# Performance work log

Measured on AMD Instinct MI355X. Metric: run time of the kernel, lower is better.

Reference implementation:

```python
import jax, jax.numpy as jnp
import numpy as np

NQ, NK, D = 8192, 8192, 128

def setup_inputs() -> dict:
    key = jax.random.key(0)
    kq, kk, kv = jax.random.split(key, 3)
    Q = jax.random.normal(kq, (NQ, D), dtype=jnp.float32)
    K = jax.random.normal(kk, (NK, D), dtype=jnp.float32)
    V = jax.random.normal(kv, (NK, D), dtype=jnp.float32)
    return {"Q": Q, "K": K, "V": V}

def reference(Q, K, V):
    d_k = K.shape[-1]
    scores = jnp.matmul(Q, K.T) / jnp.sqrt(jnp.asarray(d_k, Q.dtype))  # [NQ, NK]
    probs = jax.nn.softmax(scores, axis=-1)  # softmax over key axis
    return jnp.matmul(probs, V)  # [NQ, D]
```

## Files before the change

### kernel.cpp

```cpp
#include <hip/hip_runtime.h>
#include <hip/hip_bf16.h>

#define NQ 8192
#define NK 8192
#define DH 128
#define KVBLK 64
#define SLICES 8
#define TILES (NK / SLICES / KVBLK)
#define LOG2E 1.44269504088896340736f

typedef __attribute__((ext_vector_type(8))) short short8;
typedef __attribute__((ext_vector_type(8))) unsigned short ushort8v;
typedef __attribute__((ext_vector_type(16))) float f32x16;

static __device__ __forceinline__ unsigned short f2bf(float x){
  unsigned u = __builtin_bit_cast(unsigned, x);
  u += 0x7FFFu + ((u >> 16) & 1u);
  return (unsigned short)(u >> 16);
}

static __device__ __forceinline__ void gload_lds16(const void* g, void* l){
  __builtin_amdgcn_global_load_lds((const __attribute__((address_space(1))) void*)g,
                                   (__attribute__((address_space(3))) void*)l,
                                   16, 0, 0);
}

__global__ __launch_bounds__(512) void prep_q(const float4* __restrict__ Q4,
                                              ushort8v* __restrict__ Qb8)
{
  int i = blockIdx.x * 512 + threadIdx.x;
  const float s = 0.08838834764831844f;
  float4 a = Q4[2 * i], b = Q4[2 * i + 1];
  ushort8v o;
  o[0]=f2bf(a.x*s); o[1]=f2bf(a.y*s); o[2]=f2bf(a.z*s); o[3]=f2bf(a.w*s);
  o[4]=f2bf(b.x*s); o[5]=f2bf(b.y*s); o[6]=f2bf(b.z*s); o[7]=f2bf(b.w*s);
  Qb8[i] = o;
}

__global__ __launch_bounds__(512) void prep_kv(const float* __restrict__ K,
                                               const float* __restrict__ V,
                                               unsigned char* __restrict__ Kt,
                                               unsigned char* __restrict__ Vt)
{
  __shared__ float vs[KVBLK * DH];
  const int tile = blockIdx.x;
  const int tid  = threadIdx.x;

  const float4* Vg = (const float4*)(V + (size_t)tile * KVBLK * DH);
  float4* vs4 = (float4*)vs;
#pragma unroll
  for (int k = 0; k < 4; ++k) vs4[tid + k * 512] = Vg[tid + k * 512];

  unsigned char* Ktb = Kt + (size_t)tile * 16384;
  const float* Kg = K + (size_t)tile * KVBLK * DH;
#pragma unroll
  for (int k = 0; k < 2; ++k){
    int task = tid + k * 512;
    int kv = task >> 4, d0 = (task & 15) * 8;
    const float4* p = (const float4*)(Kg + kv * DH + d0);
    float4 a = p[0], b = p[1];
    ushort8v o;
    o[0]=f2bf(a.x); o[1]=f2bf(a.y); o[2]=f2bf(a.z); o[3]=f2bf(a.w);
    o[4]=f2bf(b.x); o[5]=f2bf(b.y); o[6]=f2bf(b.z); o[7]=f2bf(b.w);
    int addr = (kv * 256 + d0 * 2) ^ ((kv & 7) << 4);
    *(ushort8v*)(Ktb + addr) = o;
  }
  __syncthreads();

  unsigned char* Vtb = Vt + (size_t)tile * 16384;
#pragma unroll
  for (int k = 0; k < 2; ++k){
    int task = tid + k * 512;
    int d = task >> 3, mm = (task >> 1) & 3, h = task & 1;
    int kvb = mm * 16 + h * 4;
    ushort8v o;
    o[0]=f2bf(vs[(kvb+0)*DH + d]); o[1]=f2bf(vs[(kvb+1)*DH + d]);
    o[2]=f2bf(vs[(kvb+2)*DH + d]); o[3]=f2bf(vs[(kvb+3)*DH + d]);
    o[4]=f2bf(vs[(kvb+8)*DH + d]); o[5]=f2bf(vs[(kvb+9)*DH + d]);
    o[6]=f2bf(vs[(kvb+10)*DH + d]); o[7]=f2bf(vs[(kvb+11)*DH + d]);
    int addr = (d * 128 + (mm * 16 + h * 8) * 2) ^ ((d & 7) << 4);
    *(ushort8v*)(Vtb + addr) = o;
  }
}

__global__ __launch_bounds__(512, 2) void attn_kernel(
    const unsigned short* __restrict__ Qb,
    const unsigned char* __restrict__ Kt,
    const unsigned char* __restrict__ Vt,
    float* __restrict__ Opart, float* __restrict__ Mpart, float* __restrict__ Lpart)
{
  __shared__ unsigned char lK[2][16384];
  __shared__ unsigned char lV[2][16384];

  const int tid  = threadIdx.x;
  const int wave = tid >> 6;
  const int lane = tid & 63;
  const int l32  = lane & 31;
  const int h    = lane >> 5;
  const int bq    = blockIdx.x >> 3;
  const int slice = blockIdx.x & 7;
  const int qrow0 = bq * 256 + wave * 32;
  const size_t tile0 = (size_t)slice * TILES;
  const int kx = (l32 & 7) << 4;

  short8 qf[8];
  {
    const unsigned short* qp = Qb + (size_t)(qrow0 + l32) * DH + 8 * h;
#pragma unroll
    for (int m = 0; m < 8; ++m) qf[m] = *(const short8*)(qp + 16 * m);
  }

  f32x16 acc[4];
#pragma unroll
  for (int c = 0; c < 4; ++c)
#pragma unroll
    for (int r = 0; r < 16; ++r) acc[c][r] = 0.0f;
  float m_run = -3.0e38f, l_run = 0.0f;

  auto stage = [&](int buf, int t){
    if (wave < 4){
      const unsigned char* g = Kt + (tile0 + t) * 16384 + (wave * 64 + lane) * 16;
      unsigned char* l = &lK[buf][(wave * 64 + lane) * 16];
#pragma unroll
      for (int j = 0; j < 4; ++j) gload_lds16(g + j * 4096, l + j * 4096);
    } else {
      const unsigned char* g = Vt + (tile0 + t) * 16384 + ((wave - 4) * 64 + lane) * 16;
      unsigned char* l = &lV[buf][((wave - 4) * 64 + lane) * 16];
#pragma unroll
      for (int j = 0; j < 4; ++j) gload_lds16(g + j * 4096, l + j * 4096);
    }
  };

  stage(0, 0);
  __syncthreads();
  int cur = 0;

  for (int t = 0; t < TILES; ++t){
    if (t + 1 < TILES) stage(cur ^ 1, t + 1);

    const unsigned char* Kb = lK[cur];
    const unsigned char* Vb = lV[cur];

    f32x16 S0, S1;
#pragma unroll
    for (int r = 0; r < 16; ++r){ S0[r] = 0.0f; S1[r] = 0.0f; }
    __builtin_amdgcn_s_setprio(1);
#pragma unroll
    for (int m = 0; m < 8; ++m){
      short8 a = *(const short8*)(Kb + l32 * 256 + ((32 * m + 16 * h) ^ kx));
      short8 b = *(const short8*)(Kb + 8192 + l32 * 256 + ((32 * m + 16 * h) ^ kx));
      S0 = __builtin_amdgcn_mfma_f32_32x32x16_bf16(a, qf[m], S0, 0, 0, 0);
      S1 = __builtin_amdgcn_mfma_f32_32x32x16_bf16(b, qf[m], S1, 0, 0, 0);
    }
    __builtin_amdgcn_s_setprio(0);

    float pm = -3.0e38f;
#pragma unroll
    for (int r = 0; r < 16; ++r){
      pm = fmaxf(pm, S0[r]);
      pm = fmaxf(pm, S1[r]);
    }
    pm = fmaxf(pm, __shfl_xor(pm, 32, 64));

    if (!__all(pm <= m_run + 8.0f)){
      float mnew = fmaxf(m_run, pm);
      float rs = exp2f((m_run - mnew) * LOG2E);
      l_run *= rs; m_run = mnew;
#pragma unroll
      for (int r = 0; r < 16; ++r){
        float f = __shfl(rs, (r & 3) + 8 * (r >> 2) + 4 * h, 64);
#pragma unroll
        for (int c = 0; c < 4; ++c) acc[c][r] *= f;
      }
    }

    float p0[16], p1[16], psum = 0.0f;
#pragma unroll
    for (int r = 0; r < 16; ++r){
      p0[r] = exp2f((S0[r] - m_run) * LOG2E);
      p1[r] = exp2f((S1[r] - m_run) * LOG2E);
      psum += p0[r] + p1[r];
    }
    psum += __shfl_xor(psum, 32, 64);
    l_run += psum;

    short8 pa[4];
#pragma unroll
    for (int e = 0; e < 8; ++e){
      pa[0][e] = (short)f2bf(p0[e]);
      pa[1][e] = (short)f2bf(p0[8 + e]);
      pa[2][e] = (short)f2bf(p1[e]);
      pa[3][e] = (short)f2bf(p1[8 + e]);
    }

    __builtin_amdgcn_s_setprio(1);
#pragma unroll
    for (int c = 0; c < 4; ++c){
      const unsigned char* vrow = Vb + (32 * c + l32) * 128;
#pragma unroll
      for (int mm = 0; mm < 4; ++mm){
        short8 vfr = *(const short8*)(vrow + ((mm * 32 + 16 * h) ^ kx));
        acc[c] = __builtin_amdgcn_mfma_f32_32x32x16_bf16(pa[mm], vfr, acc[c], 0, 0, 0);
      }
    }
    __builtin_amdgcn_s_setprio(0);

    __syncthreads();
    cur ^= 1;
  }

  if (lane < 32){
    Mpart[(size_t)slice * NQ + qrow0 + lane] = m_run;
    Lpart[(size_t)slice * NQ + qrow0 + lane] = l_run;
  }
#pragma unroll
  for (int c = 0; c < 4; ++c)
#pragma unroll
    for (int r = 0; r < 16; ++r){
      int q = qrow0 + (r & 3) + 8 * (r >> 2) + 4 * h;
      Opart[((size_t)slice * NQ + q) * DH + 32 * c + l32] = acc[c][r];
    }
}

__global__ __launch_bounds__(256) void combine_kernel(
    const float4* __restrict__ Op4, const float* __restrict__ Mp,
    const float* __restrict__ Lp, float4* __restrict__ Out4)
{
  const int q  = blockIdx.x * 8 + (threadIdx.x >> 5);
  const int dd = threadIdx.x & 31;

  float ms[SLICES], M = -3.0e38f;
#pragma unroll
  for (int s = 0; s < SLICES; ++s){ ms[s] = Mp[s * NQ + q]; M = fmaxf(M, ms[s]); }
  float L = 0.0f, w[SLICES];
#pragma unroll
  for (int s = 0; s < SLICES; ++s){
    w[s] = exp2f((ms[s] - M) * LOG2E);
    L += Lp[s * NQ + q] * w[s];
  }
  float4 o = make_float4(0.f, 0.f, 0.f, 0.f);
#pragma unroll
  for (int s = 0; s < SLICES; ++s){
    float4 v = Op4[((size_t)s * NQ + q) * 32 + dd];
    o.x += w[s] * v.x; o.y += w[s] * v.y; o.z += w[s] * v.z; o.w += w[s] * v.w;
  }
  float inv = 1.0f / L;
  Out4[(size_t)q * 32 + dd] = make_float4(o.x * inv, o.y * inv, o.z * inv, o.w * inv);
}

extern "C" void kernel_launch(void* const* d_in, const int* in_sizes, int n_in,
                              void* d_out, int out_size, void* d_ws, size_t ws_size,
                              hipStream_t stream)
{
  const float* Q = (const float*)d_in[0];
  const float* K = (const float*)d_in[1];
  const float* V = (const float*)d_in[2];

  unsigned char* ws = (unsigned char*)d_ws;
  const size_t MB2 = (size_t)NQ * DH * 2;
  unsigned short* Qb = (unsigned short*)ws;
  unsigned char*  Kt = ws + MB2;
  unsigned char*  Vt = ws + 2 * MB2;
  float* Mp = (float*)(ws + 3 * MB2);
  float* Lp = Mp + (size_t)SLICES * NQ;
  float* Op = Lp + (size_t)SLICES * NQ;

  prep_q<<<NQ * DH / 8 / 512, 512, 0, stream>>>((const float4*)Q, (ushort8v*)Qb);
  prep_kv<<<NK / KVBLK, 512, 0, stream>>>(K, V, Kt, Vt);
  attn_kernel<<<(NQ / 256) * SLICES, 512, 0, stream>>>(Qb, Kt, Vt, Op, Mp, Lp);
  combine_kernel<<<NQ / 8, 256, 0, stream>>>((const float4*)Op, Mp, Lp, (float4*)d_out);
}
```

Baseline: 125.2 us.

## Give each wave 64 query rows, halve KV tiles, double slices, store bf16 partials

Each wave now computes two 32-row query blocks that share every K and V fragment loaded from LDS. This halves LDS reads per MFMA. KV tiles shrink to 32 rows and the key split grows to 16 slices with 256-thread blocks, and the staging and swizzle layout are rewritten to match. The log2e factor is folded into the Q prescale so the per-element multiplies in the exponentials go away. Partial outputs are written as bf16 to cut workspace traffic into the combine kernel, which adds rounding error and doubles the number of partials to merge.

```diff
diff --git a/kernel.cpp b/kernel.cpp
--- a/kernel.cpp
+++ b/kernel.cpp
@@ -4,10 +4,11 @@
 #define NQ 8192
 #define NK 8192
 #define DH 128
-#define KVBLK 64
-#define SLICES 8
-#define TILES (NK / SLICES / KVBLK)
-#define LOG2E 1.44269504088896340736f
+#define KVBLK 32
+#define SLICES 16
+#define KVPER (NK / SLICES)
+#define TILES (KVPER / KVBLK)
+#define NTILES (NK / KVBLK)
 
 typedef __attribute__((ext_vector_type(8))) short short8;
 typedef __attribute__((ext_vector_type(8))) unsigned short ushort8v;
@@ -18,7 +19,10 @@
   u += 0x7FFFu + ((u >> 16) & 1u);
   return (unsigned short)(u >> 16);
 }
-
+static __device__ __forceinline__ float bf2f(unsigned short x){
+  unsigned u = ((unsigned)x) << 16;
+  return __builtin_bit_cast(float, u);
+}
 static __device__ __forceinline__ void gload_lds16(const void* g, void* l){
   __builtin_amdgcn_global_load_lds((const __attribute__((address_space(1))) void*)g,
                                    (__attribute__((address_space(3))) void*)l,
@@ -29,7 +33,7 @@
                                               ushort8v* __restrict__ Qb8)
 {
   int i = blockIdx.x * 512 + threadIdx.x;
-  const float s = 0.08838834764831844f;
+  const float s = 1.4426950408889634f * 0.08838834764831844f;
   float4 a = Q4[2 * i], b = Q4[2 * i + 1];
   ushort8v o;
   o[0]=f2bf(a.x*s); o[1]=f2bf(a.y*s); o[2]=f2bf(a.z*s); o[3]=f2bf(a.w*s);
@@ -37,7 +41,7 @@
   Qb8[i] = o;
 }
 
-__global__ __launch_bounds__(512) void prep_kv(const float* __restrict__ K,
+__global__ __launch_bounds__(256) void prep_kv(const float* __restrict__ K,
                                                const float* __restrict__ V,
                                                unsigned char* __restrict__ Kt,
                                                unsigned char* __restrict__ Vt)
@@ -49,13 +53,13 @@
   const float4* Vg = (const float4*)(V + (size_t)tile * KVBLK * DH);
   float4* vs4 = (float4*)vs;
 #pragma unroll
-  for (int k = 0; k < 4; ++k) vs4[tid + k * 512] = Vg[tid + k * 512];
-
-  unsigned char* Ktb = Kt + (size_t)tile * 16384;
+  for (int k = 0; k < 4; ++k) vs4[tid + k * 256] = Vg[tid + k * 256];
+
+  unsigned char* Ktb = Kt + (size_t)tile * 8192;
   const float* Kg = K + (size_t)tile * KVBLK * DH;
 #pragma unroll
-  for (int k = 0; k < 2; ++k){
-    int task = tid + k * 512;
+  for (int k2 = 0; k2 < 2; ++k2){
+    int task = tid + k2 * 256;
     int kv = task >> 4, d0 = (task & 15) * 8;
     const float4* p = (const float4*)(Kg + kv * DH + d0);
     float4 a = p[0], b = p[1];
@@ -67,68 +71,73 @@
   }
   __syncthreads();
 
-  unsigned char* Vtb = Vt + (size_t)tile * 16384;
-#pragma unroll
-  for (int k = 0; k < 2; ++k){
-    int task = tid + k * 512;
-    int d = task >> 3, mm = (task >> 1) & 3, h = task & 1;
-    int kvb = mm * 16 + h * 4;
+  unsigned char* Vtb = Vt + (size_t)tile * 8192;
+#pragma unroll
+  for (int k2 = 0; k2 < 2; ++k2){
+    int task = tid + k2 * 256;
+    int d = task >> 2, mm = (task >> 1) & 1, hh = task & 1;
+    int kvb = mm * 16 + hh * 4;
     ushort8v o;
-    o[0]=f2bf(vs[(kvb+0)*DH + d]); o[1]=f2bf(vs[(kvb+1)*DH + d]);
-    o[2]=f2bf(vs[(kvb+2)*DH + d]); o[3]=f2bf(vs[(kvb+3)*DH + d]);
-    o[4]=f2bf(vs[(kvb+8)*DH + d]); o[5]=f2bf(vs[(kvb+9)*DH + d]);
+    o[0]=f2bf(vs[(kvb+0)*DH + d]);  o[1]=f2bf(vs[(kvb+1)*DH + d]);
+    o[2]=f2bf(vs[(kvb+2)*DH + d]);  o[3]=f2bf(vs[(kvb+3)*DH + d]);
+    o[4]=f2bf(vs[(kvb+8)*DH + d]);  o[5]=f2bf(vs[(kvb+9)*DH + d]);
     o[6]=f2bf(vs[(kvb+10)*DH + d]); o[7]=f2bf(vs[(kvb+11)*DH + d]);
-    int addr = (d * 128 + (mm * 16 + h * 8) * 2) ^ ((d & 7) << 4);
+    int addr = d * 64 + ((mm * 32 + hh * 16) ^ ((d & 3) << 4));
     *(ushort8v*)(Vtb + addr) = o;
   }
 }
 
-__global__ __launch_bounds__(512, 2) void attn_kernel(
+__global__ __launch_bounds__(256, 2) void attn_kernel(
     const unsigned short* __restrict__ Qb,
     const unsigned char* __restrict__ Kt,
     const unsigned char* __restrict__ Vt,
-    float* __restrict__ Opart, float* __restrict__ Mpart, float* __restrict__ Lpart)
-{
-  __shared__ unsigned char lK[2][16384];
-  __shared__ unsigned char lV[2][16384];
+    unsigned short* __restrict__ Opart,
+    float* __restrict__ Mpart, float* __restrict__ Lpart)
+{
+  __shared__ unsigned char lK[2][8192];
+  __shared__ unsigned char lV[2][8192];
 
   const int tid  = threadIdx.x;
+  const int lane = tid & 63;
   const int wave = tid >> 6;
-  const int lane = tid & 63;
   const int l32  = lane & 31;
   const int h    = lane >> 5;
-  const int bq    = blockIdx.x >> 3;
-  const int slice = blockIdx.x & 7;
-  const int qrow0 = bq * 256 + wave * 32;
-  const size_t tile0 = (size_t)slice * TILES;
+  const int bq    = blockIdx.x >> 4;
+  const int slice = blockIdx.x & 15;
+  const int qrow0 = bq * 256 + wave * 64;
+  const int tile0 = slice * TILES;
   const int kx = (l32 & 7) << 4;
-
-  short8 qf[8];
+  const int vx = (l32 & 3) << 4;
+
+  const unsigned char* gkb = Kt + (size_t)tile0 * 8192;
+  const unsigned char* gvb = Vt + (size_t)tile0 * 8192;
+
+  short8 qfA[8], qfB[8];
   {
-    const unsigned short* qp = Qb + (size_t)(qrow0 + l32) * DH + 8 * h;
-#pragma unroll
-    for (int m = 0; m < 8; ++m) qf[m] = *(const short8*)(qp + 16 * m);
-  }
-
-  f32x16 acc[4];
+    const unsigned short* qa = Qb + (size_t)(qrow0 + l32) * DH + 8 * h;
+    const unsigned short* qb = qa + 32 * DH;
+#pragma unroll
+    for (int m = 0; m < 8; ++m){
+      qfA[m] = *(const short8*)(qa + 16 * m);
+      qfB[m] = *(const short8*)(qb + 16 * m);
+    }
+  }
+
+  f32x16 accA[4], accB[4];
 #pragma unroll
   for (int c = 0; c < 4; ++c)
 #pragma unroll
-    for (int r = 0; r < 16; ++r) acc[c][r] = 0.0f;
-  float m_run = -3.0e38f, l_run = 0.0f;
-
+    for (int r = 0; r < 16; ++r){ accA[c][r] = 0.0f; accB[c][r] = 0.0f; }
+  float mA = -3.0e38f, lA = 0.0f, mB = -3.0e38f, lB = 0.0f;
+
+  const int soff = tid * 16;
   auto stage = [&](int buf, int t){
-    if (wave < 4){
-      const unsigned char* g = Kt + (tile0 + t) * 16384 + (wave * 64 + lane) * 16;
-      unsigned char* l = &lK[buf][(wave * 64 + lane) * 16];
-#pragma unroll
-      for (int j = 0; j < 4; ++j) gload_lds16(g + j * 4096, l + j * 4096);
-    } else {
-      const unsigned char* g = Vt + (tile0 + t) * 16384 + ((wave - 4) * 64 + lane) * 16;
-      unsigned char* l = &lV[buf][((wave - 4) * 64 + lane) * 16];
-#pragma unroll
-      for (int j = 0; j < 4; ++j) gload_lds16(g + j * 4096, l + j * 4096);
-    }
+    const unsigned char* gk = gkb + (size_t)t * 8192;
+    const unsigned char* gv = gvb + (size_t)t * 8192;
+    gload_lds16(gk + soff,        &lK[buf][soff]);
+    gload_lds16(gk + soff + 4096, &lK[buf][soff + 4096]);
+    gload_lds16(gv + soff,        &lV[buf][soff]);
+    gload_lds16(gv + soff + 4096, &lV[buf][soff + 4096]);
   };
 
   stage(0, 0);
@@ -141,67 +150,80 @@
     const unsigned char* Kb = lK[cur];
     const unsigned char* Vb = lV[cur];
 
-    f32x16 S0, S1;
-#pragma unroll
-    for (int r = 0; r < 16; ++r){ S0[r] = 0.0f; S1[r] = 0.0f; }
+    f32x16 SA, SB;
+#pragma unroll
+    for (int r = 0; r < 16; ++r){ SA[r] = 0.0f; SB[r] = 0.0f; }
     __builtin_amdgcn_s_setprio(1);
 #pragma unroll
     for (int m = 0; m < 8; ++m){
-      short8 a = *(const short8*)(Kb + l32 * 256 + ((32 * m + 16 * h) ^ kx));
-      short8 b = *(const short8*)(Kb + 8192 + l32 * 256 + ((32 * m + 16 * h) ^ kx));
-      S0 = __builtin_amdgcn_mfma_f32_32x32x16_bf16(a, qf[m], S0, 0, 0, 0);
-      S1 = __builtin_amdgcn_mfma_f32_32x32x16_bf16(b, qf[m], S1, 0, 0, 0);
+      short8 kf = *(const short8*)(Kb + l32 * 256 + ((32 * m + 16 * h) ^ kx));
+      SA = __builtin_amdgcn_mfma_f32_32x32x16_bf16(kf, qfA[m], SA, 0, 0, 0);
+      SB = __builtin_amdgcn_mfma_f32_32x32x16_bf16(kf, qfB[m], SB, 0, 0, 0);
     }
     __builtin_amdgcn_s_setprio(0);
 
-    float pm = -3.0e38f;
+    float pmA = -3.0e38f, pmB = -3.0e38f;
 #pragma unroll
     for (int r = 0; r < 16; ++r){
-      pm = fmaxf(pm, S0[r]);
-      pm = fmaxf(pm, S1[r]);
-    }
-    pm = fmaxf(pm, __shfl_xor(pm, 32, 64));
-
-    if (!__all(pm <= m_run + 8.0f)){
-      float mnew = fmaxf(m_run, pm);
-      float rs = exp2f((m_run - mnew) * LOG2E);
-      l_run *= rs; m_run = mnew;
+      pmA = fmaxf(pmA, SA[r]);
+      pmB = fmaxf(pmB, SB[r]);
+    }
+    pmA = fmaxf(pmA, __shfl_xor(pmA, 32, 64));
+    pmB = fmaxf(pmB, __shfl_xor(pmB, 32, 64));
+
+    if (!__all(pmA <= mA + 8.0f)){
+      float mnew = fmaxf(mA, pmA);
+      float rs = exp2f(mA - mnew);
+      lA *= rs; mA = mnew;
 #pragma unroll
       for (int r = 0; r < 16; ++r){
         float f = __shfl(rs, (r & 3) + 8 * (r >> 2) + 4 * h, 64);
 #pragma unroll
-        for (int c = 0; c < 4; ++c) acc[c][r] *= f;
+        for (int c = 0; c < 4; ++c) accA[c][r] *= f;
       }
     }
-
-    float p0[16], p1[16], psum = 0.0f;
+    if (!__all(pmB <= mB + 8.0f)){
+      float mnew = fmaxf(mB, pmB);
+      float rs = exp2f(mB - mnew);
+      lB *= rs; mB = mnew;
+#pragma unroll
+      for (int r = 0; r < 16; ++r){
+        float f = __shfl(rs, (r & 3) + 8 * (r >> 2) + 4 * h, 64);
+#pragma unroll
+        for (int c = 0; c < 4; ++c) accB[c][r] *= f;
+      }
+    }
+
+    float psA = 0.0f, psB = 0.0f;
 #pragma unroll
     for (int r = 0; r < 16; ++r){
-      p0[r] = exp2f((S0[r] - m_run) * LOG2E);
-      p1[r] = exp2f((S1[r] - m_run) * LOG2E);
-      psum += p0[r] + p1[r];
-    }
-    psum += __shfl_xor(psum, 32, 64);
-    l_run += psum;
-
-    short8 pa[4];
+      SA[r] = exp2f(SA[r] - mA);
+      SB[r] = exp2f(SB[r] - mB);
+      psA += SA[r]; psB += SB[r];
+    }
+    psA += __shfl_xor(psA, 32, 64);
+    psB += __shfl_xor(psB, 32, 64);
+    lA += psA; lB += psB;
+
+    short8 paA[2], paB[2];
 #pragma unroll
     for (int e = 0; e < 8; ++e){
-      pa[0][e] = (short)f2bf(p0[e]);
-      pa[1][e] = (short)f2bf(p0[8 + e]);
-      pa[2][e] = (short)f2bf(p1[e]);
-      pa[3][e] = (short)f2bf(p1[8 + e]);
+      paA[0][e] = (short)f2bf(SA[e]);
+      paA[1][e] = (short)f2bf(SA[8 + e]);
+      paB[0][e] = (short)f2bf(SB[e]);
+      paB[1][e] = (short)f2bf(SB[8 + e]);
     }
 
     __builtin_amdgcn_s_setprio(1);
 #pragma unroll
     for (int c = 0; c < 4; ++c){
-      const unsigned char* vrow = Vb + (32 * c + l32) * 128;
-#pragma unroll
-      for (int mm = 0; mm < 4; ++mm){
-        short8 vfr = *(const short8*)(vrow + ((mm * 32 + 16 * h) ^ kx));
-        acc[c] = __builtin_amdgcn_mfma_f32_32x32x16_bf16(pa[mm], vfr, acc[c], 0, 0, 0);
-      }
+      const unsigned char* vrow = Vb + (32 * c + l32) * 64;
+      short8 v0 = *(const short8*)(vrow + ((16 * h) ^ vx));
+      short8 v1 = *(const short8*)(vrow + ((32 + 16 * h) ^ vx));
+      accA[c] = __builtin_amdgcn_mfma_f32_32x32x16_bf16(paA[0], v0, accA[c], 0, 0, 0);
+      accB[c] = __builtin_amdgcn_mfma_f32_32x32x16_bf16(paB[0], v0, accB[c], 0, 0, 0);
+      accA[c] = __builtin_amdgcn_mfma_f32_32x32x16_bf16(paA[1], v1, accA[c], 0, 0, 0);
+      accB[c] = __builtin_amdgcn_mfma_f32_32x32x16_bf16(paB[1], v1, accB[c], 0, 0, 0);
     }
     __builtin_amdgcn_s_setprio(0);
 
@@ -209,43 +231,53 @@
     cur ^= 1;
   }
 
-  if (lane < 32){
-    Mpart[(size_t)slice * NQ + qrow0 + lane] = m_run;
-    Lpart[(size_t)slice * NQ + qrow0 + lane] = l_run;
-  }
+  if (h == 0){
+    Mpart[slice * NQ + qrow0 + l32] = mA;
+    Lpart[slice * NQ + qrow0 + l32] = lA;
+    Mpart[slice * NQ + qrow0 + 32 + l32] = mB;
+    Lpart[slice * NQ + qrow0 + 32 + l32] = lB;
+  }
+  const size_t obase = ((size_t)slice * NQ + qrow0) * DH;
 #pragma unroll
   for (int c = 0; c < 4; ++c)
 #pragma unroll
     for (int r = 0; r < 16; ++r){
-      int q = qrow0 + (r & 3) + 8 * (r >> 2) + 4 * h;
-      Opart[((size_t)slice * NQ + q) * DH + 32 * c + l32] = acc[c][r];
+      int q = (r & 3) + 8 * (r >> 2) + 4 * h;
+      Opart[obase + (size_t)q * DH + 32 * c + l32]        = f2bf(accA[c][r]);
+      Opart[obase + (size_t)(32 + q) * DH + 32 * c + l32] = f2bf(accB[c][r]);
     }
 }
 
 __global__ __launch_bounds__(256) void combine_kernel(
-    const float4* __restrict__ Op4, const float* __restrict__ Mp,
-    const float* __restrict__ Lp, float4* __restrict__ Out4)
-{
-  const int q  = blockIdx.x * 8 + (threadIdx.x >> 5);
-  const int dd = threadIdx.x & 31;
+    const unsigned short* __restrict__ Op, const float* __restrict__ Mp,
+    const float* __restrict__ Lp, float* __restrict__ Out)
+{
+  const int idx = blockIdx.x * 256 + threadIdx.x;
+  const int q  = idx >> 4;
+  const int d8 = (idx & 15) * 8;
 
   float ms[SLICES], M = -3.0e38f;
 #pragma unroll
   for (int s = 0; s < SLICES; ++s){ ms[s] = Mp[s * NQ + q]; M = fmaxf(M, ms[s]); }
-  float L = 0.0f, w[SLICES];
+  float w[SLICES], L = 0.0f;
 #pragma unroll
   for (int s = 0; s < SLICES; ++s){
-    w[s] = exp2f((ms[s] - M) * LOG2E);
+    w[s] = exp2f(ms[s] - M);
     L += Lp[s * NQ + q] * w[s];
   }
-  float4 o = make_float4(0.f, 0.f, 0.f, 0.f);
+  float o[8] = {0,0,0,0,0,0,0,0};
 #pragma unroll
   for (int s = 0; s < SLICES; ++s){
-    float4 v = Op4[((size_t)s * NQ + q) * 32 + dd];
-    o.x += w[s] * v.x; o.y += w[s] * v.y; o.z += w[s] * v.z; o.w += w[s] * v.w;
+    ushort8v v = *(const ushort8v*)(Op + ((size_t)s * NQ + q) * DH + d8);
+    float ww = w[s];
+#pragma unroll
+    for (int e = 0; e < 8; ++e) o[e] += ww * bf2f(v[e]);
   }
   float inv = 1.0f / L;
-  Out4[(size_t)q * 32 + dd] = make_float4(o.x * inv, o.y * inv, o.z * inv, o.w * inv);
+  float4 o0 = make_float4(o[0]*inv, o[1]*inv, o[2]*inv, o[3]*inv);
+  float4 o1 = make_float4(o[4]*inv, o[5]*inv, o[6]*inv, o[7]*inv);
+  float4* dst = (float4*)(Out + (size_t)q * DH + d8);
+  dst[0] = o0; dst[1] = o1;
 }
 
 extern "C" void kernel_launch(void* const* d_in, const int* in_sizes, int n_in,
@@ -263,10 +295,10 @@
   unsigned char*  Vt = ws + 2 * MB2;
   float* Mp = (float*)(ws + 3 * MB2);
   float* Lp = Mp + (size_t)SLICES * NQ;
-  float* Op = Lp + (size_t)SLICES * NQ;
+  unsigned short* Op = (unsigned short*)(Lp + (size_t)SLICES * NQ);
 
   prep_q<<<NQ * DH / 8 / 512, 512, 0, stream>>>((const float4*)Q, (ushort8v*)Qb);
-  prep_kv<<<NK / KVBLK, 512, 0, stream>>>(K, V, Kt, Vt);
-  attn_kernel<<<(NQ / 256) * SLICES, 512, 0, stream>>>(Qb, Kt, Vt, Op, Mp, Lp);
-  combine_kernel<<<NQ / 8, 256, 0, stream>>>((const float4*)Op, Mp, Lp, (float4*)d_out);
-}
+  prep_kv<<<NTILES, 256, 0, stream>>>(K, V, Kt, Vt);
+  attn_kernel<<<(NQ / 256) * SLICES, 256, 0, stream>>>(Qb, Kt, Vt, Op, Mp, Lp);
+  combine_kernel<<<NQ * 16 / 256, 256, 0, stream>>>(Op, Mp, Lp, (float*)d_out);
+}
```

Measured after the change: 126.9 us. No clear change (+1.4%).
